# Kernel tuning notes

Hardware: AMD Instinct MI355X
Metric: run time of the kernel (lower is better)

The kernel has to match this reference:

```python
import jax, jax.numpy as jnp
import numpy as np

B, L, D, H, DFF = 4, 2048, 1024, 16, 4096
DH = D // H
INF = 1e12


def setup_inputs() -> dict:
    key = jax.random.key(0)
    ks = jax.random.split(key, 20)
    s = lambda fan_in: 1.0 / np.sqrt(fan_in)
    inp = {
        'x': jax.random.normal(ks[0], (B, L, D), jnp.float32),
        'mask': jax.random.bernoulli(ks[1], 0.1, (B, 1, 1, L)),
        'wq': jax.random.normal(ks[2], (D, D), jnp.float32) * s(D),
        'bq': jnp.zeros((D,), jnp.float32),
        'wk': jax.random.normal(ks[3], (D, D), jnp.float32) * s(D),
        'bk': jnp.zeros((D,), jnp.float32),
        'wv': jax.random.normal(ks[4], (D, D), jnp.float32) * s(D),
        'bv': jnp.zeros((D,), jnp.float32),
        'wo': jax.random.normal(ks[5], (D, D), jnp.float32) * s(D),
        'bo': jnp.zeros((D,), jnp.float32),
        'w1': jax.random.normal(ks[6], (D, DFF), jnp.float32) * s(D),
        'b1': jnp.zeros((DFF,), jnp.float32),
        'w2': jax.random.normal(ks[7], (DFF, D), jnp.float32) * s(DFF),
        'b2': jnp.zeros((D,), jnp.float32),
        'g1': jnp.ones((D,), jnp.float32),
        'beta1': jnp.zeros((D,), jnp.float32),
        'g2': jnp.ones((D,), jnp.float32),
        'beta2': jnp.zeros((D,), jnp.float32),
    }
    return inp


def _layernorm(x, g, b, eps=1e-5):
    mu = jnp.mean(x, axis=-1, keepdims=True)
    var = jnp.mean(jnp.square(x - mu), axis=-1, keepdims=True)
    return (x - mu) * jax.lax.rsqrt(var + eps) * g + b


def reference(x, mask, wq, bq, wk, bk, wv, bv, wo, bo, w1, b1, w2, b2, g1, beta1, g2, beta2):
    # --- self attention ---
    def split_heads(t):  # [B,L,D] -> [B,H,L,DH]
        return t.reshape(B, L, H, DH).transpose(0, 2, 1, 3)

    Q = split_heads(x @ wq + bq)
    K = split_heads(x @ wk + bk)
    V = split_heads(x @ wv + bv)

    dots = jnp.einsum('bhqd,bhkd->bhqk', Q, K) / np.sqrt(DH)  # [B,H,L,L]
    dots = jnp.where(mask, -INF, dots)
    attn = jax.nn.softmax(dots, axis=-1)
    out = jnp.einsum('bhqk,bhkd->bhqd', attn, V)
    out = out.transpose(0, 2, 1, 3).reshape(B, L, D)
    out = out @ wo + bo

    x = _layernorm(x + out, g1, beta1)

    # --- feed forward ---
    h = jax.nn.relu(x @ w1 + b1)
    ff = h @ w2 + b2
    x = _layernorm(x + ff, g2, beta2)
    return x
```

## Files before the change

kernel.cpp:

```cpp
#include <hip/hip_runtime.h>
#include <hip/hip_bf16.h>

#define B_   4
#define L_   2048
#define D_   1024
#define H_   16
#define DH_  64
#define DFF_ 4096
#define M_   (B_ * L_)

typedef __attribute__((ext_vector_type(8))) short bf16x8;
typedef __attribute__((ext_vector_type(4))) float f32x4;

#define GLOAD16(gp, lp)                                                       \
  __builtin_amdgcn_global_load_lds(                                           \
      (const __attribute__((address_space(1))) unsigned int*)(gp),            \
      (__attribute__((address_space(3))) unsigned int*)(lp), 16, 0, 0)

#if __has_builtin(__builtin_amdgcn_exp2f)
#define EXP2F(x) __builtin_amdgcn_exp2f(x)
#else
#define EXP2F(x) exp2f(x)
#endif

__device__ __forceinline__ float bf2f(unsigned short u) {
  return __uint_as_float(((unsigned)u) << 16);
}

__global__ void prep_and_transpose(
    const float4* __restrict__ x4, ushort4* __restrict__ xb4,
    const unsigned int* __restrict__ mraw, float* __restrict__ maskf,
    const float* __restrict__ bq, const float* __restrict__ bk,
    const float* __restrict__ bv, float* __restrict__ biasc,
    const float* __restrict__ wq, const float* __restrict__ wk,
    const float* __restrict__ wv, const float* __restrict__ wo,
    const float* __restrict__ w1, const float* __restrict__ w2,
    __hip_bfloat16* __restrict__ WQT, __hip_bfloat16* __restrict__ WKT,
    __hip_bfloat16* __restrict__ WVT, __hip_bfloat16* __restrict__ WOT,
    __hip_bfloat16* __restrict__ W1T, __hip_bfloat16* __restrict__ W2T) {
  const int id = blockIdx.x;
  if (id < 8192) {
    const int i = id * 256 + threadIdx.x;
    float4 v = x4[i];
    __hip_bfloat16 a = __float2bfloat16(v.x);
    __hip_bfloat16 b = __float2bfloat16(v.y);
    __hip_bfloat16 c = __float2bfloat16(v.z);
    __hip_bfloat16 d = __float2bfloat16(v.w);
    ushort4 o;
    o.x = *reinterpret_cast<unsigned short*>(&a);
    o.y = *reinterpret_cast<unsigned short*>(&b);
    o.z = *reinterpret_cast<unsigned short*>(&c);
    o.w = *reinterpret_cast<unsigned short*>(&d);
    xb4[i] = o;
    return;
  }
  if (id < 8224) {
    __shared__ int flags[2];
    if (threadIdx.x < 2) flags[threadIdx.x] = 0;
    __syncthreads();
    int nf32 = 0, n01 = 0;
    for (int i = threadIdx.x; i < 2048; i += 256) {
      unsigned w = mraw[i];
      if (w != 0u && w != 0x3f800000u) nf32 = 1;
      if (w > 1u) n01 = 1;
    }
    if (nf32) atomicOr(&flags[0], 1);
    if (n01)  atomicOr(&flags[1], 1);
    __syncthreads();
    const int mode = (!flags[0]) ? 0 : ((!flags[1]) ? 1 : 2);
    const int mi = (id - 8192) * 256 + threadIdx.x;
    if (mi < B_ * L_) {
      bool mk;
      if (mode == 0)      mk = reinterpret_cast<const float*>(mraw)[mi] != 0.f;
      else if (mode == 1) mk = reinterpret_cast<const int*>(mraw)[mi] != 0;
      else                mk = reinterpret_cast<const unsigned char*>(mraw)[mi] != 0;
      maskf[mi] = mk ? -1e12f : -32.0f;
    }
    if (id == 8192) {
#pragma unroll
      for (int j = 0; j < 4; ++j) {
        const int c = j * 256 + threadIdx.x;
        biasc[c] = bq[c];
        biasc[D_ + c] = bk[c];
        biasc[2 * D_ + c] = bv[c];
      }
    }
    return;
  }
  __shared__ float t[32][33];
  const int wid = id - 8224;
  const float* W;
  __hip_bfloat16* Wt;
  int K, N, rem;
  if (wid < 4096) {
    const int which = wid >> 10;
    W  = which == 0 ? wq : which == 1 ? wk : which == 2 ? wv : wo;
    Wt = which == 0 ? WQT : which == 1 ? WKT : which == 2 ? WVT : WOT;
    K = D_; N = D_; rem = wid & 1023;
  } else if (wid < 8192) {
    W = w1; Wt = W1T; K = D_; N = DFF_; rem = wid - 4096;
  } else {
    W = w2; Wt = W2T; K = DFF_; N = D_; rem = wid - 8192;
  }
  const int ntx = N >> 5;
  const int n0 = (rem % ntx) * 32, k0 = (rem / ntx) * 32;
  const int tx = threadIdx.x & 31, ty = threadIdx.x >> 5;
#pragma unroll
  for (int i = 0; i < 4; ++i)
    t[ty + i * 8][tx] = W[(size_t)(k0 + ty + i * 8) * N + n0 + tx];
  __syncthreads();
#pragma unroll
  for (int i = 0; i < 4; ++i)
    Wt[(size_t)(n0 + ty + i * 8) * K + k0 + tx] =
        __float2bfloat16(t[tx][ty + i * 8]);
}

__global__ void transpose_v(const __hip_bfloat16* __restrict__ Vin,
                            __hip_bfloat16* __restrict__ Vt) {
  __shared__ __hip_bfloat16 t[32][33];
  const int l0 = blockIdx.x * 32, d0 = blockIdx.y * 32, b = blockIdx.z;
  const int tx = threadIdx.x, ty = threadIdx.y;
#pragma unroll
  for (int i = 0; i < 4; ++i)
    t[ty + i * 8][tx] = Vin[(size_t)(b * L_ + l0 + ty + i * 8) * D_ + d0 + tx];
  __syncthreads();
#pragma unroll
  for (int i = 0; i < 4; ++i) {
    int d = d0 + ty + i * 8;
    Vt[(size_t)(b * D_ + d) * L_ + l0 + tx] = t[tx][ty + i * 8];
  }
}

#define STAGE8(matptr, stride, ldsbase, tile, kh, rowbase)                    \
  {                                                                           \
    _Pragma("unroll")                                                         \
    for (int j_ = 0; j_ < 2; ++j_) {                                          \
      const int s_ = j_ * 512 + tid;                                          \
      const int row_ = s_ >> 2;                                               \
      const int q_ = (s_ & 3) ^ ((row_ >> 1) & 3);                            \
      GLOAD16(&matptr[(size_t)((rowbase) + row_) * (stride) + (tile) * 64 +   \
                      (kh) * 32 + q_ * 8],                                    \
              (ldsbase) + (j_ * 512 + (w << 6)) * 16);                        \
    }                                                                         \
  }

#define PHASE8(bufoff, rh, ks, dovm, ...)                                     \
  {                                                                           \
    if ((rh) == 0) {                                                          \
      _Pragma("unroll")                                                       \
      for (int j = 0; j < 4; ++j) {                                           \
        const int br = wn * 64 + j * 16 + r16;                                \
        bfr[j] = *reinterpret_cast<const bf16x8*>(                            \
            ldsB + (bufoff) + (ks) * 16384 + br * 64 +                        \
            ((hi * 16) ^ (((br >> 1) & 3) << 4)));                            \
      }                                                                       \
    }                                                                         \
    bf16x8 af[4];                                                             \
    _Pragma("unroll")                                                         \
    for (int i = 0; i < 4; ++i) {                                             \
      const int ar = wm * 128 + (rh) * 64 + i * 16 + r16;                     \
      af[i] = *reinterpret_cast<const bf16x8*>(                               \
          ldsA + (bufoff) + (ks) * 16384 + ar * 64 +                          \
          ((hi * 16) ^ (((ar >> 1) & 3) << 4)));                              \
    }                                                                         \
    __VA_ARGS__;                                                              \
    __builtin_amdgcn_s_barrier();                                             \
    asm volatile("s_waitcnt lgkmcnt(0)" ::: "memory");                        \
    __builtin_amdgcn_sched_barrier(0);                                        \
    __builtin_amdgcn_s_setprio(1);                                            \
    _Pragma("unroll")                                                         \
    for (int i = 0; i < 4; ++i)                                               \
      _Pragma("unroll")                                                       \
      for (int j = 0; j < 4; ++j)                                             \
        acc[(rh) * 4 + i][j] = __builtin_amdgcn_mfma_f32_16x16x32_bf16(       \
            af[i], bfr[j], acc[(rh) * 4 + i][j], 0, 0, 0);                    \
    __builtin_amdgcn_s_setprio(0);                                            \
    if (dovm) {                                                               \
      asm volatile("s_waitcnt vmcnt(4)" ::: "memory");                        \
      __builtin_amdgcn_sched_barrier(0);                                      \
    }                                                                         \
    __builtin_amdgcn_s_barrier();                                             \
  }

template <int EP>
__global__ __launch_bounds__(512, 1) void gemm8(
    const __hip_bfloat16* __restrict__ A, const __hip_bfloat16* __restrict__ Bt,
    const float* __restrict__ bias, void* __restrict__ out,
    int M, int N, int K, int lda, int ldb) {
  __shared__ __align__(16) char lds8[131072];
  char* const ldsA = lds8;
  char* const ldsB = lds8 + 65536;

  const int tid = threadIdx.x;
  const int lane = tid & 63;
  const int w = tid >> 6;
  const int wm = w >> 2;
  const int wn = w & 3;
  const int r16 = lane & 15;
  const int hi = lane >> 4;

  const int nwg = gridDim.x;
  const int orig = blockIdx.x;
  const int swz = (orig & 7) * (nwg >> 3) + (orig >> 3);

  int bm, bn, kh = 0;
  const __hip_bfloat16* Ap = A;
  const __hip_bfloat16* Bp = Bt;
  if (EP == 4) {
    kh = swz & 1;
    const int rest = swz >> 1;
    bm = (rest & 31) * 256;
    bn = (rest >> 5) * 256;
    Ap += (size_t)kh * K;
    Bp += (size_t)kh * K;
  } else {
    bm = (swz & 31) * 256;
    bn = (swz >> 5) * 256;
  }

  f32x4 acc[8][4];
#pragma unroll
  for (int i = 0; i < 8; ++i)
#pragma unroll
    for (int j = 0; j < 4; ++j) acc[i][j] = (f32x4){0.f, 0.f, 0.f, 0.f};
  bf16x8 bfr[4];

  const int nkt = K >> 6;
  const int nit = nkt >> 1;

  STAGE8(Ap, lda, ldsA, 0, 0, bm);
  STAGE8(Bp, ldb, ldsB, 0, 0, bn);
  STAGE8(Ap, lda, ldsA + 16384, 0, 1, bm);
  STAGE8(Bp, ldb, ldsB + 16384, 0, 1, bn);
  STAGE8(Ap, lda, ldsA + 32768, 1, 0, bm);
  STAGE8(Bp, ldb, ldsB + 32768, 1, 0, bn);
  asm volatile("s_waitcnt vmcnt(4)" ::: "memory");
  __builtin_amdgcn_sched_barrier(0);
  __builtin_amdgcn_s_barrier();

  for (int it = 0; it < nit; ++it) {
    const int kt = it * 2;
    const bool hn = (it + 1) < nit;
    PHASE8(0, 0, 0, 0, STAGE8(Ap, lda, ldsA + 49152, kt + 1, 1, bm));
    PHASE8(0, 1, 0, 0, STAGE8(Bp, ldb, ldsB + 49152, kt + 1, 1, bn));
    PHASE8(0, 0, 1, 0, if (hn) STAGE8(Ap, lda, ldsA, kt + 2, 0, bm));
    PHASE8(0, 1, 1, 1, if (hn) STAGE8(Bp, ldb, ldsB, kt + 2, 0, bn));
    PHASE8(32768, 0, 0, 0, if (hn) STAGE8(Ap, lda, ldsA + 16384, kt + 2, 1, bm));
    PHASE8(32768, 1, 0, 0, if (hn) STAGE8(Bp, ldb, ldsB + 16384, kt + 2, 1, bn));
    PHASE8(32768, 0, 1, 0, if (hn) STAGE8(Ap, lda, ldsA + 32768, kt + 3, 0, bm));
    PHASE8(32768, 1, 1, 1, if (hn) STAGE8(Bp, ldb, ldsB + 32768, kt + 3, 0, bn));
  }

#pragma unroll
  for (int ri = 0; ri < 8; ++ri) {
#pragma unroll
    for (int j = 0; j < 4; ++j) {
      const int col = bn + wn * 64 + j * 16 + r16;
      const float bv = (EP == 4) ? 0.f : bias[col];
#pragma unroll
      for (int r = 0; r < 4; ++r) {
        const int row = bm + wm * 128 + ri * 16 + hi * 4 + r;
        const float v = acc[ri][j][r] + bv;
        if (EP == 1) {
          ((__hip_bfloat16*)out)[(size_t)row * N + col] =
              __float2bfloat16(v > 0.f ? v : 0.f);
        } else if (EP == 3) {
          __hip_bfloat16* outp =
              (__hip_bfloat16*)out + (size_t)(col >> 10) * (M_ * D_);
          outp[(size_t)row * 1024 + (col & 1023)] = __float2bfloat16(v);
        } else {
          __hip_bfloat16* outp =
              (__hip_bfloat16*)out + (size_t)kh * ((size_t)M * N);
          outp[(size_t)row * N + col] = __float2bfloat16(v);
        }
      }
    }
  }
}

template <int EP>
__global__ __launch_bounds__(256) void gemm_bt(
    const __hip_bfloat16* __restrict__ A, const __hip_bfloat16* __restrict__ Bt,
    const float* __restrict__ bias, const float* __restrict__ res,
    void* __restrict__ out, int M, int N, int K) {
  __shared__ __align__(16) char As[128 * 64];
  __shared__ __align__(16) char Bs[128 * 64];
  const int tid = threadIdx.x;
  const int lane = tid & 63;
  const int w = tid >> 6;
  const int wm = w >> 1, wn = w & 1;
  const int bm = blockIdx.x * 128;
  const int bn = blockIdx.y * 128;
  const int r16 = lane & 15;
  const int hi = lane >> 4;

  f32x4 acc[4][4];
#pragma unroll
  for (int m = 0; m < 4; ++m)
#pragma unroll
    for (int n = 0; n < 4; ++n) acc[m][n] = (f32x4){0.f, 0.f, 0.f, 0.f};

  for (int k0 = 0; k0 < K; k0 += 32) {
    __syncthreads();
#pragma unroll
    for (int c = 0; c < 2; ++c) {
      const int seg = c * 256 + tid;
      const int row = seg >> 2;
      const int csl = (seg & 3) ^ (row & 3);
      GLOAD16(&A[(size_t)(bm + row) * K + k0 + csl * 8],
              As + (c * 256 + w * 64) * 16);
      GLOAD16(&Bt[(size_t)(bn + row) * K + k0 + csl * 8],
              Bs + (c * 256 + w * 64) * 16);
    }
    __syncthreads();

    bf16x8 af[4], bfr[4];
#pragma unroll
    for (int m = 0; m < 4; ++m) {
      const int arow = wm * 64 + m * 16 + r16;
      af[m] = *reinterpret_cast<const bf16x8*>(
          As + arow * 64 + ((hi * 16) ^ ((arow & 3) << 4)));
    }
#pragma unroll
    for (int n = 0; n < 4; ++n) {
      const int brow = wn * 64 + n * 16 + r16;
      bfr[n] = *reinterpret_cast<const bf16x8*>(
          Bs + brow * 64 + ((hi * 16) ^ ((brow & 3) << 4)));
    }
#pragma unroll
    for (int m = 0; m < 4; ++m)
#pragma unroll
      for (int n = 0; n < 4; ++n)
        acc[m][n] = __builtin_amdgcn_mfma_f32_16x16x32_bf16(af[m], bfr[n],
                                                            acc[m][n], 0, 0, 0);
  }

  const int rg = hi * 4;
#pragma unroll
  for (int m = 0; m < 4; ++m) {
#pragma unroll
    for (int n = 0; n < 4; ++n) {
      const int col = bn + wn * 64 + n * 16 + r16;
      const float bv = bias[col];
#pragma unroll
      for (int r = 0; r < 4; ++r) {
        const int row = bm + wm * 64 + m * 16 + rg + r;
        const size_t idx = (size_t)row * N + col;
        float v = acc[m][n][r] + bv;
        if (EP == 0) {
          ((__hip_bfloat16*)out)[idx] = __float2bfloat16(v);
        } else {
          ((float*)out)[idx] = v + res[idx];
        }
      }
    }
  }
}

__global__ __launch_bounds__(256) void attn_kernel(
    const __hip_bfloat16* __restrict__ Qg, const __hip_bfloat16* __restrict__ Kg,
    const __hip_bfloat16* __restrict__ VTg,
    const float* __restrict__ maskf,
    __hip_bfloat16* __restrict__ Og) {
  __shared__ __align__(16) char Kl[64 * 128];
  __shared__ __align__(16) char Vl[64 * 128];
  __shared__ __align__(16) char Pl[4][32 * 128];
  __shared__ float maskb[64];

  const int tid = threadIdx.x;
  const int lane = tid & 63;
  const int w = tid >> 6;
  const int hi = lane >> 4;
  const int r16 = lane & 15;
  const int swzk = (r16 & 7) << 4;

  const int nwg = gridDim.x;
  const int orig = blockIdx.x;
  const int swb = (orig & 7) * (nwg >> 3) + (orig >> 3);
  const int qb = swb & 15;
  const int bh = swb >> 4;
  const int b = bh >> 4;
  const int h = bh & 15;
  const int qbase = qb * 128 + w * 32;

  const float C = 0.18033688011112042f;
  const short ob = (short)0x3f80;
  const bf16x8 vone = {ob, ob, ob, ob, ob, ob, ob, ob};

  bf16x8 qf[2][2];
#pragma unroll
  for (int m = 0; m < 2; ++m)
#pragma unroll
    for (int ks = 0; ks < 2; ++ks)
      qf[m][ks] = *reinterpret_cast<const bf16x8*>(
          &Qg[(size_t)(b * L_ + qbase + m * 16 + r16) * D_ + h * DH_ +
              ks * 32 + hi * 8]);

  f32x4 o[2][4];
  f32x4 oden[2];
#pragma unroll
  for (int m = 0; m < 2; ++m) {
    oden[m] = (f32x4){0.f, 0.f, 0.f, 0.f};
#pragma unroll
    for (int nd = 0; nd < 4; ++nd) o[m][nd] = (f32x4){0.f, 0.f, 0.f, 0.f};
  }

  char* const Plw = Pl[w];

  for (int kv0 = 0; kv0 < L_; kv0 += 64) {
    __syncthreads();
#pragma unroll
    for (int c = 0; c < 2; ++c) {
      const int seg = c * 256 + tid;
      const int row = seg >> 3;
      const int csl = (seg & 7) ^ (row & 7);
      GLOAD16(&Kg[(size_t)(b * L_ + kv0 + row) * D_ + h * DH_ + csl * 8],
              Kl + (c * 256 + w * 64) * 16);
      GLOAD16(&VTg[(size_t)(b * D_ + h * DH_ + row) * L_ + kv0 + csl * 8],
              Vl + (c * 256 + w * 64) * 16);
    }
    if (tid < 64) maskb[tid] = maskf[(size_t)b * L_ + kv0 + tid];
    __syncthreads();

    f32x4 sacc[2][4];
#pragma unroll
    for (int m = 0; m < 2; ++m)
#pragma unroll
      for (int n = 0; n < 4; ++n) sacc[m][n] = (f32x4){0.f, 0.f, 0.f, 0.f};
    __builtin_amdgcn_s_setprio(1);
#pragma unroll
    for (int n = 0; n < 4; ++n) {
      const int krow = n * 16 + r16;
#pragma unroll
      for (int ks = 0; ks < 2; ++ks) {
        const bf16x8 kf = *reinterpret_cast<const bf16x8*>(
            Kl + krow * 128 + ((ks * 64 + hi * 16) ^ swzk));
#pragma unroll
        for (int m = 0; m < 2; ++m)
          sacc[m][n] = __builtin_amdgcn_mfma_f32_16x16x32_bf16(
              kf, qf[m][ks], sacc[m][n], 0, 0, 0);
      }
    }
    __builtin_amdgcn_s_setprio(0);

    float4 mv[4];
#pragma unroll
    for (int n = 0; n < 4; ++n)
      mv[n] = *reinterpret_cast<const float4*>(&maskb[n * 16 + hi * 4]);
#pragma unroll
    for (int m = 0; m < 2; ++m) {
      const int prow = m * 16 + r16;
#pragma unroll
      for (int n = 0; n < 4; ++n) {
        const float e0 = EXP2F(fmaf(sacc[m][n][0], C, mv[n].x));
        const float e1 = EXP2F(fmaf(sacc[m][n][1], C, mv[n].y));
        const float e2 = EXP2F(fmaf(sacc[m][n][2], C, mv[n].z));
        const float e3 = EXP2F(fmaf(sacc[m][n][3], C, mv[n].w));
        union { unsigned long long u; unsigned short us[4]; } pk;
        __hip_bfloat16 t0 = __float2bfloat16(e0);
        __hip_bfloat16 t1 = __float2bfloat16(e1);
        __hip_bfloat16 t2 = __float2bfloat16(e2);
        __hip_bfloat16 t3 = __float2bfloat16(e3);
        pk.us[0] = *reinterpret_cast<unsigned short*>(&t0);
        pk.us[1] = *reinterpret_cast<unsigned short*>(&t1);
        pk.us[2] = *reinterpret_cast<unsigned short*>(&t2);
        pk.us[3] = *reinterpret_cast<unsigned short*>(&t3);
        *reinterpret_cast<unsigned long long*>(
            Plw + prow * 128 + ((n * 32 + hi * 8) ^ swzk)) = pk.u;
      }
    }

    bf16x8 pa[2][2];
#pragma unroll
    for (int m = 0; m < 2; ++m)
#pragma unroll
      for (int ks = 0; ks < 2; ++ks)
        pa[m][ks] = *reinterpret_cast<const bf16x8*>(
            Plw + (m * 16 + r16) * 128 + ((ks * 64 + hi * 16) ^ swzk));
    __builtin_amdgcn_s_setprio(1);
#pragma unroll
    for (int m = 0; m < 2; ++m)
#pragma unroll
      for (int ks = 0; ks < 2; ++ks)
        oden[m] = __builtin_amdgcn_mfma_f32_16x16x32_bf16(pa[m][ks], vone,
                                                          oden[m], 0, 0, 0);
#pragma unroll
    for (int nd = 0; nd < 4; ++nd) {
      const int vrow = nd * 16 + r16;
#pragma unroll
      for (int ks = 0; ks < 2; ++ks) {
        const bf16x8 vb = *reinterpret_cast<const bf16x8*>(
            Vl + vrow * 128 + ((ks * 64 + hi * 16) ^ swzk));
#pragma unroll
        for (int m = 0; m < 2; ++m)
          o[m][nd] = __builtin_amdgcn_mfma_f32_16x16x32_bf16(pa[m][ks], vb,
                                                             o[m][nd], 0, 0, 0);
      }
    }
    __builtin_amdgcn_s_setprio(0);
  }

#pragma unroll
  for (int m = 0; m < 2; ++m) {
#pragma unroll
    for (int r = 0; r < 4; ++r) {
      const float ir = 1.f / oden[m][r];
      const int q = qbase + m * 16 + hi * 4 + r;
#pragma unroll
      for (int nd = 0; nd < 4; ++nd)
        Og[(size_t)(b * L_ + q) * D_ + h * DH_ + nd * 16 + r16] =
            __float2bfloat16(o[m][nd][r] * ir);
    }
  }
}

__global__ __launch_bounds__(256) void layernorm_kernel(
    const float* __restrict__ in, const float* __restrict__ g,
    const float* __restrict__ be, float* __restrict__ outf,
    __hip_bfloat16* __restrict__ outb) {
  const int row = blockIdx.x;
  const int tid = threadIdx.x;
  const float4 v = reinterpret_cast<const float4*>(in + (size_t)row * D_)[tid];
  float s = v.x + v.y + v.z + v.w;
  float ss = v.x * v.x + v.y * v.y + v.z * v.z + v.w * v.w;
#pragma unroll
  for (int off = 1; off < 64; off <<= 1) {
    s += __shfl_xor(s, off, 64);
    ss += __shfl_xor(ss, off, 64);
  }
  __shared__ float red[8];
  const int w = tid >> 6, lane = tid & 63;
  if (lane == 0) { red[w] = s; red[4 + w] = ss; }
  __syncthreads();
  s = red[0] + red[1] + red[2] + red[3];
  ss = red[4] + red[5] + red[6] + red[7];
  const float mu = s * (1.f / D_);
  const float rs = rsqrtf(ss * (1.f / D_) - mu * mu + 1e-5f);
  const float4 gv = reinterpret_cast<const float4*>(g)[tid];
  const float4 bv = reinterpret_cast<const float4*>(be)[tid];
  float4 ov;
  ov.x = (v.x - mu) * rs * gv.x + bv.x;
  ov.y = (v.y - mu) * rs * gv.y + bv.y;
  ov.z = (v.z - mu) * rs * gv.z + bv.z;
  ov.w = (v.w - mu) * rs * gv.w + bv.w;
  reinterpret_cast<float4*>(outf + (size_t)row * D_)[tid] = ov;
  if (outb) {
    __hip_bfloat16 t[4] = {__float2bfloat16(ov.x), __float2bfloat16(ov.y),
                           __float2bfloat16(ov.z), __float2bfloat16(ov.w)};
    *reinterpret_cast<uint2*>(&outb[(size_t)row * D_ + tid * 4]) =
        *reinterpret_cast<const uint2*>(t);
  }
}

__global__ __launch_bounds__(256) void ln_addres(
    const __hip_bfloat16* __restrict__ OP, const float* __restrict__ x,
    const float* __restrict__ g, const float* __restrict__ be,
    float* __restrict__ outf, __hip_bfloat16* __restrict__ outb) {
  const int row = blockIdx.x;
  const int tid = threadIdx.x;
  const ushort4 a4 = reinterpret_cast<const ushort4*>(OP + (size_t)row * D_)[tid];
  const float4 xr = reinterpret_cast<const float4*>(x + (size_t)row * D_)[tid];
  float4 v;
  v.x = bf2f(a4.x) + xr.x;
  v.y = bf2f(a4.y) + xr.y;
  v.z = bf2f(a4.z) + xr.z;
  v.w = bf2f(a4.w) + xr.w;
  float s = v.x + v.y + v.z + v.w;
  float ss = v.x * v.x + v.y * v.y + v.z * v.z + v.w * v.w;
#pragma unroll
  for (int off = 1; off < 64; off <<= 1) {
    s += __shfl_xor(s, off, 64);
    ss += __shfl_xor(ss, off, 64);
  }
  __shared__ float red[8];
  const int w = tid >> 6, lane = tid & 63;
  if (lane == 0) { red[w] = s; red[4 + w] = ss; }
  __syncthreads();
  s = red[0] + red[1] + red[2] + red[3];
  ss = red[4] + red[5] + red[6] + red[7];
  const float mu = s * (1.f / D_);
  const float rs = rsqrtf(ss * (1.f / D_) - mu * mu + 1e-5f);
  const float4 gv = reinterpret_cast<const float4*>(g)[tid];
  const float4 bv = reinterpret_cast<const float4*>(be)[tid];
  float4 ov;
  ov.x = (v.x - mu) * rs * gv.x + bv.x;
  ov.y = (v.y - mu) * rs * gv.y + bv.y;
  ov.z = (v.z - mu) * rs * gv.z + bv.z;
  ov.w = (v.w - mu) * rs * gv.w + bv.w;
  reinterpret_cast<float4*>(outf + (size_t)row * D_)[tid] = ov;
  __hip_bfloat16 t[4] = {__float2bfloat16(ov.x), __float2bfloat16(ov.y),
                         __float2bfloat16(ov.z), __float2bfloat16(ov.w)};
  *reinterpret_cast<uint2*>(&outb[(size_t)row * D_ + tid * 4]) =
      *reinterpret_cast<const uint2*>(t);
}

__global__ __launch_bounds__(256) void ln_addres_sk(
    const __hip_bfloat16* __restrict__ P0, const __hip_bfloat16* __restrict__ P1,
    const float* __restrict__ x, const float* __restrict__ bo,
    const float* __restrict__ g, const float* __restrict__ be,
    float* __restrict__ outf, __hip_bfloat16* __restrict__ outb) {
  const int row = blockIdx.x;
  const int tid = threadIdx.x;
  const ushort4 a4 = reinterpret_cast<const ushort4*>(P0 + (size_t)row * D_)[tid];
  const ushort4 b4 = reinterpret_cast<const ushort4*>(P1 + (size_t)row * D_)[tid];
  const float4 xr = reinterpret_cast<const float4*>(x + (size_t)row * D_)[tid];
  const float4 bb = reinterpret_cast<const float4*>(bo)[tid];
  float4 v;
  v.x = bf2f(a4.x) + bf2f(b4.x) + xr.x + bb.x;
  v.y = bf2f(a4.y) + bf2f(b4.y) + xr.y + bb.y;
  v.z = bf2f(a4.z) + bf2f(b4.z) + xr.z + bb.z;
  v.w = bf2f(a4.w) + bf2f(b4.w) + xr.w + bb.w;
  float s = v.x + v.y + v.z + v.w;
  float ss = v.x * v.x + v.y * v.y + v.z * v.z + v.w * v.w;
#pragma unroll
  for (int off = 1; off < 64; off <<= 1) {
    s += __shfl_xor(s, off, 64);
    ss += __shfl_xor(ss, off, 64);
  }
  __shared__ float red[8];
  const int w = tid >> 6, lane = tid & 63;
  if (lane == 0) { red[w] = s; red[4 + w] = ss; }
  __syncthreads();
  s = red[0] + red[1] + red[2] + red[3];
  ss = red[4] + red[5] + red[6] + red[7];
  const float mu = s * (1.f / D_);
  const float rs = rsqrtf(ss * (1.f / D_) - mu * mu + 1e-5f);
  const float4 gv = reinterpret_cast<const float4*>(g)[tid];
  const float4 bv = reinterpret_cast<const float4*>(be)[tid];
  float4 ov;
  ov.x = (v.x - mu) * rs * gv.x + bv.x;
  ov.y = (v.y - mu) * rs * gv.y + bv.y;
  ov.z = (v.z - mu) * rs * gv.z + bv.z;
  ov.w = (v.w - mu) * rs * gv.w + bv.w;
  reinterpret_cast<float4*>(outf + (size_t)row * D_)[tid] = ov;
  __hip_bfloat16 t[4] = {__float2bfloat16(ov.x), __float2bfloat16(ov.y),
                         __float2bfloat16(ov.z), __float2bfloat16(ov.w)};
  *reinterpret_cast<uint2*>(&outb[(size_t)row * D_ + tid * 4]) =
      *reinterpret_cast<const uint2*>(t);
}

__global__ __launch_bounds__(256) void combine_ln2(
    const __hip_bfloat16* __restrict__ P0, const __hip_bfloat16* __restrict__ P1,
    const float* __restrict__ res, const float* __restrict__ b2,
    const float* __restrict__ g, const float* __restrict__ be,
    float* __restrict__ out) {
  const int row = blockIdx.x;
  const int tid = threadIdx.x;
  const ushort4 a4 =
      reinterpret_cast<const ushort4*>(P0 + (size_t)row * D_)[tid];
  const ushort4 b4 =
      reinterpret_cast<const ushort4*>(P1 + (size_t)row * D_)[tid];
  const float4 rr = reinterpret_cast<const float4*>(res + (size_t)row * D_)[tid];
  const float4 bb = reinterpret_cast<const float4*>(b2)[tid];
  float4 v;
  v.x = bf2f(a4.x) + bf2f(b4.x) + rr.x + bb.x;
  v.y = bf2f(a4.y) + bf2f(b4.y) + rr.y + bb.y;
  v.z = bf2f(a4.z) + bf2f(b4.z) + rr.z + bb.z;
  v.w = bf2f(a4.w) + bf2f(b4.w) + rr.w + bb.w;
  float s = v.x + v.y + v.z + v.w;
  float ss = v.x * v.x + v.y * v.y + v.z * v.z + v.w * v.w;
#pragma unroll
  for (int off = 1; off < 64; off <<= 1) {
    s += __shfl_xor(s, off, 64);
    ss += __shfl_xor(ss, off, 64);
  }
  __shared__ float red[8];
  const int w = tid >> 6, lane = tid & 63;
  if (lane == 0) { red[w] = s; red[4 + w] = ss; }
  __syncthreads();
  s = red[0] + red[1] + red[2] + red[3];
  ss = red[4] + red[5] + red[6] + red[7];
  const float mu = s * (1.f / D_);
  const float rs = rsqrtf(ss * (1.f / D_) - mu * mu + 1e-5f);
  const float4 gv = reinterpret_cast<const float4*>(g)[tid];
  const float4 bv = reinterpret_cast<const float4*>(be)[tid];
  float4 ov;
  ov.x = (v.x - mu) * rs * gv.x + bv.x;
  ov.y = (v.y - mu) * rs * gv.y + bv.y;
  ov.z = (v.z - mu) * rs * gv.z + bv.z;
  ov.w = (v.w - mu) * rs * gv.w + bv.w;
  reinterpret_cast<float4*>(out + (size_t)row * D_)[tid] = ov;
}

extern "C" void kernel_launch(void* const* d_in, const int* in_sizes, int n_in,
                              void* d_out, int out_size, void* d_ws,
                              size_t ws_size, hipStream_t stream) {
  (void)in_sizes; (void)n_in; (void)out_size;
  const float* x   = (const float*)d_in[0];
  const void*  msk = d_in[1];
  const float* wq  = (const float*)d_in[2];
  const float* bq  = (const float*)d_in[3];
  const float* wk  = (const float*)d_in[4];
  const float* bk  = (const float*)d_in[5];
  const float* wv  = (const float*)d_in[6];
  const float* bv  = (const float*)d_in[7];
  const float* wo  = (const float*)d_in[8];
  const float* bo  = (const float*)d_in[9];
  const float* w1  = (const float*)d_in[10];
  const float* b1  = (const float*)d_in[11];
  const float* w2  = (const float*)d_in[12];
  const float* b2  = (const float*)d_in[13];
  const float* g1  = (const float*)d_in[14];
  const float* be1 = (const float*)d_in[15];
  const float* g2  = (const float*)d_in[16];
  const float* be2 = (const float*)d_in[17];

  char* ws = (char*)d_ws;
  float*          MASKF = (float*)(ws + 256);
  float*          BIASC = (float*)(ws + 40960);
  __hip_bfloat16* XB    = (__hip_bfloat16*)(ws + 65536);
  __hip_bfloat16* WQT   = (__hip_bfloat16*)(ws + 16842752);
  __hip_bfloat16* WKT   = (__hip_bfloat16*)(ws + 18939904);
  __hip_bfloat16* WVT   = (__hip_bfloat16*)(ws + 21037056);
  __hip_bfloat16* WOT   = (__hip_bfloat16*)(ws + 23134208);
  __hip_bfloat16* W1T   = (__hip_bfloat16*)(ws + 25231360);
  __hip_bfloat16* W2T   = (__hip_bfloat16*)(ws + 33619968);
  __hip_bfloat16* QB    = (__hip_bfloat16*)(ws + 42008576);
  __hip_bfloat16* KB    = (__hip_bfloat16*)(ws + 58785792);
  __hip_bfloat16* VB    = (__hip_bfloat16*)(ws + 75563008);
  __hip_bfloat16* OB    = (__hip_bfloat16*)(ws + 92340224);
  __hip_bfloat16* HB    = QB;
  __hip_bfloat16* VT    = (__hip_bfloat16*)(ws + 109117440);
  __hip_bfloat16* OP    = VT;
  float*          R1    = (float*)(ws + 125894656);
  __hip_bfloat16* P0    = (__hip_bfloat16*)(ws + 159449088);
  __hip_bfloat16* P1    = (__hip_bfloat16*)(ws + 176226304);
  float*          OUT   = (float*)d_out;
  const bool use_splitk = ws_size >= 193003520ull;

  prep_and_transpose<<<20512, 256, 0, stream>>>(
      (const float4*)x, (ushort4*)XB, (const unsigned int*)msk, MASKF,
      bq, bk, bv, BIASC, wq, wk, wv, wo, w1, w2,
      WQT, WKT, WVT, WOT, W1T, W2T);

  gemm8<3><<<dim3((M_ / 256) * (3 * D_ / 256)), 512, 0, stream>>>(
      XB, WQT, BIASC, QB, M_, 3 * D_, D_, D_, D_);

  transpose_v<<<dim3(L_ / 32, D_ / 32, B_), dim3(32, 8), 0, stream>>>(VB, VT);
  attn_kernel<<<dim3(B_ * H_ * (L_ / 128)), 256, 0, stream>>>(QB, KB, VT, MASKF, OB);

  if (use_splitk) {
    gemm8<4><<<dim3((M_ / 256) * (D_ / 256) * 2), 512, 0, stream>>>(
        OB, WOT, nullptr, P0, M_, D_, D_ / 2, D_, D_);
    ln_addres_sk<<<M_, 256, 0, stream>>>(P0, P1, x, bo, g1, be1, R1, XB);
  } else {
    gemm_bt<0><<<dim3(M_ / 128, D_ / 128), 256, 0, stream>>>(OB, WOT, bo, nullptr, OP, M_, D_, D_);
    ln_addres<<<M_, 256, 0, stream>>>(OP, x, g1, be1, R1, XB);
  }

  gemm8<1><<<dim3((M_ / 256) * (DFF_ / 256)), 512, 0, stream>>>(
      XB, W1T, b1, HB, M_, DFF_, D_, D_, D_);
  if (use_splitk) {
    gemm8<4><<<dim3((M_ / 256) * (D_ / 256) * 2), 512, 0, stream>>>(
        HB, W2T, nullptr, P0, M_, D_, DFF_ / 2, DFF_, DFF_);
    combine_ln2<<<M_, 256, 0, stream>>>(P0, P1, R1, b2, g2, be2, OUT);
  } else {
    gemm_bt<2><<<dim3(M_ / 128, D_ / 128), 256, 0, stream>>>(HB, W2T, b2, R1, OUT, M_, D_, DFF_);
    layernorm_kernel<<<M_, 256, 0, stream>>>(OUT, g2, be2, OUT, nullptr);
  }
}
```

Before: 410.5 us.

## Double-buffer K/V tiles in attention and prefetch mask into registers

The attention kernel now keeps two LDS buffers for K and V and issues the global-to-LDS loads for the next 64-key tile before computing on the current one, so only one barrier per iteration is needed. The per-tile mask is prefetched straight from global memory into registers instead of going through shared memory. The goal is to hide K/V load latency behind the MFMA work. In exchange LDS use per block doubles for K/V, which could lower occupancy, and the s_waitcnt vmcnt(0) at the top of each iteration still waits for all outstanding loads.

```diff
diff --git a/kernel.cpp b/kernel.cpp
--- a/kernel.cpp
+++ b/kernel.cpp
@@ -362,10 +362,9 @@
     const __hip_bfloat16* __restrict__ VTg,
     const float* __restrict__ maskf,
     __hip_bfloat16* __restrict__ Og) {
-  __shared__ __align__(16) char Kl[64 * 128];
-  __shared__ __align__(16) char Vl[64 * 128];
+  __shared__ __align__(16) char Kl[2][64 * 128];
+  __shared__ __align__(16) char Vl[2][64 * 128];
   __shared__ __align__(16) char Pl[4][32 * 128];
-  __shared__ float maskb[64];
 
   const int tid = threadIdx.x;
   const int lane = tid & 63;
@@ -387,6 +386,21 @@
   const short ob = (short)0x3f80;
   const bf16x8 vone = {ob, ob, ob, ob, ob, ob, ob, ob};
 
+  const float* const mb = maskf + (size_t)b * L_;
+
+#define STAGE_KV(kvv, buf)                                                    \
+  {                                                                           \
+    _Pragma("unroll") for (int c_ = 0; c_ < 2; ++c_) {                        \
+      const int seg_ = c_ * 256 + tid;                                        \
+      const int row_ = seg_ >> 3;                                             \
+      const int csl_ = (seg_ & 7) ^ (row_ & 7);                               \
+      GLOAD16(&Kg[(size_t)(b * L_ + (kvv) + row_) * D_ + h * DH_ + csl_ * 8], \
+              Kl[buf] + (c_ * 256 + w * 64) * 16);                            \
+      GLOAD16(&VTg[(size_t)(b * D_ + h * DH_ + row_) * L_ + (kvv) + csl_ * 8],\
+              Vl[buf] + (c_ * 256 + w * 64) * 16);                            \
+    }                                                                         \
+  }
+
   bf16x8 qf[2][2];
 #pragma unroll
   for (int m = 0; m < 2; ++m)
@@ -407,20 +421,30 @@
 
   char* const Plw = Pl[w];
 
-  for (int kv0 = 0; kv0 < L_; kv0 += 64) {
-    __syncthreads();
-#pragma unroll
-    for (int c = 0; c < 2; ++c) {
-      const int seg = c * 256 + tid;
-      const int row = seg >> 3;
-      const int csl = (seg & 7) ^ (row & 7);
-      GLOAD16(&Kg[(size_t)(b * L_ + kv0 + row) * D_ + h * DH_ + csl * 8],
-              Kl + (c * 256 + w * 64) * 16);
-      GLOAD16(&VTg[(size_t)(b * D_ + h * DH_ + row) * L_ + kv0 + csl * 8],
-              Vl + (c * 256 + w * 64) * 16);
-    }
-    if (tid < 64) maskb[tid] = maskf[(size_t)b * L_ + kv0 + tid];
-    __syncthreads();
+  float4 mvn[4];
+#pragma unroll
+  for (int n = 0; n < 4; ++n)
+    mvn[n] = *reinterpret_cast<const float4*>(mb + n * 16 + hi * 4);
+  STAGE_KV(0, 0);
+
+  for (int t = 0; t < 32; ++t) {
+    const int cur = t & 1;
+    asm volatile("s_waitcnt vmcnt(0)" ::: "memory");
+    __builtin_amdgcn_sched_barrier(0);
+    __builtin_amdgcn_s_barrier();
+    __builtin_amdgcn_sched_barrier(0);
+
+    float4 mv[4];
+#pragma unroll
+    for (int n = 0; n < 4; ++n) mv[n] = mvn[n];
+
+    if (t + 1 < 32) {
+      const int kvn = (t + 1) * 64;
+#pragma unroll
+      for (int n = 0; n < 4; ++n)
+        mvn[n] = *reinterpret_cast<const float4*>(mb + kvn + n * 16 + hi * 4);
+      STAGE_KV(kvn, cur ^ 1);
+    }
 
     f32x4 sacc[2][4];
 #pragma unroll
@@ -434,7 +458,7 @@
 #pragma unroll
       for (int ks = 0; ks < 2; ++ks) {
         const bf16x8 kf = *reinterpret_cast<const bf16x8*>(
-            Kl + krow * 128 + ((ks * 64 + hi * 16) ^ swzk));
+            Kl[cur] + krow * 128 + ((ks * 64 + hi * 16) ^ swzk));
 #pragma unroll
         for (int m = 0; m < 2; ++m)
           sacc[m][n] = __builtin_amdgcn_mfma_f32_16x16x32_bf16(
@@ -443,10 +467,6 @@
     }
     __builtin_amdgcn_s_setprio(0);
 
-    float4 mv[4];
-#pragma unroll
-    for (int n = 0; n < 4; ++n)
-      mv[n] = *reinterpret_cast<const float4*>(&maskb[n * 16 + hi * 4]);
 #pragma unroll
     for (int m = 0; m < 2; ++m) {
       const int prow = m * 16 + r16;
@@ -490,7 +510,7 @@
 #pragma unroll
       for (int ks = 0; ks < 2; ++ks) {
         const bf16x8 vb = *reinterpret_cast<const bf16x8*>(
-            Vl + vrow * 128 + ((ks * 64 + hi * 16) ^ swzk));
+            Vl[cur] + vrow * 128 + ((ks * 64 + hi * 16) ^ swzk));
 #pragma unroll
         for (int m = 0; m < 2; ++m)
           o[m][nd] = __builtin_amdgcn_mfma_f32_16x16x32_bf16(pa[m][ks], vb,
@@ -512,6 +532,7 @@
             __float2bfloat16(o[m][nd][r] * ir);
     }
   }
+#undef STAGE_KV
 }
 
 __global__ __launch_bounds__(256) void layernorm_kernel(
```

New measurement: 421.6 us. 1.03x slower.
